# Performance work log

Hardware: AMD Instinct MI355X
Metric: run time of the kernel (lower is better)

The kernel has to match this reference:

```python
import jax, jax.numpy as jnp
import numpy as np
import math

D_MODEL = 1024
N_HEADS = 16
D_HEAD = D_MODEL // N_HEADS
LSR_RANK = 32
B, T = 4, 2048


def setup_inputs() -> dict:
    key = jax.random.key(0)
    ks = jax.random.split(key, 11)
    s = 1.0 / math.sqrt(D_MODEL)
    x = jax.random.normal(ks[0], (B, T, D_MODEL), dtype=jnp.float32)
    Wq = jax.random.uniform(ks[1], (D_MODEL, D_MODEL), minval=-s, maxval=s)
    bq = jax.random.uniform(ks[2], (D_MODEL,), minval=-s, maxval=s)
    Wk = jax.random.uniform(ks[3], (D_MODEL, D_MODEL), minval=-s, maxval=s)
    bk = jax.random.uniform(ks[4], (D_MODEL,), minval=-s, maxval=s)
    Wv = jax.random.uniform(ks[5], (D_MODEL, D_MODEL), minval=-s, maxval=s)
    bv = jax.random.uniform(ks[6], (D_MODEL,), minval=-s, maxval=s)
    Wo = jax.random.uniform(ks[7], (D_MODEL, D_MODEL), minval=-s, maxval=s)
    bo = jax.random.uniform(ks[8], (D_MODEL,), minval=-s, maxval=s)
    Wq_lsr = jax.random.normal(ks[9], (N_HEADS, D_HEAD, LSR_RANK)) / math.sqrt(D_HEAD)
    Wk_lsr = jax.random.normal(ks[10], (N_HEADS, D_HEAD, LSR_RANK)) / math.sqrt(D_HEAD)
    return {"x": x, "Wq": Wq, "bq": bq, "Wk": Wk, "bk": bk,
            "Wv": Wv, "bv": bv, "Wo": Wo, "bo": bo,
            "Wq_lsr": Wq_lsr, "Wk_lsr": Wk_lsr}


def reference(x, Wq, bq, Wk, bk, Wv, bv, Wo, bo, Wq_lsr, Wk_lsr):
    Bq, Tq, _ = x.shape
    # Linear projections (torch Linear: x @ W.T + b), split into heads -> (B,H,T,Dh)
    def split_heads(y):
        return y.reshape(Bq, Tq, N_HEADS, D_HEAD).transpose(0, 2, 1, 3)
    q = split_heads(x @ Wq.T + bq)
    k = split_heads(x @ Wk.T + bk)
    v = split_heads(x @ Wv.T + bv)
    # LSR: project q,k to rank-R per head
    q_lr = jnp.einsum('bhtd,hdr->bhtr', q, Wq_lsr)
    k_lr = jnp.einsum('bhtd,hdr->bhtr', k, Wk_lsr)
    scale = 1.0 / math.sqrt(max(LSR_RANK, 1))
    scores = jnp.einsum('bhir,bhjr->bhij', q_lr, k_lr) * scale  # (B,H,T,T)
    causal_mask = jnp.triu(jnp.ones((Tq, Tq), dtype=bool), k=1)
    scores = jnp.where(causal_mask, jnp.float32(-jnp.inf), scores)
    attn = jax.nn.softmax(scores, axis=-1)
    y = jnp.einsum('bhij,bhjd->bhid', attn, v)  # (B,H,T,Dh)
    y = y.transpose(0, 2, 1, 3).reshape(Bq, Tq, D_MODEL)
    return y @ Wo.T + bo
```

## Files before the change

kernel.cpp:

```cpp
#include <hip/hip_runtime.h>

#define B_  4
#define T_  2048
#define H_  16
#define DM_ 1024
#define DH_ 64
#define RK_ 32

using u16 = unsigned short;
using u32 = unsigned int;
typedef float  floatx4 __attribute__((ext_vector_type(4)));
typedef __bf16 bf16x8  __attribute__((ext_vector_type(8)));
typedef u16    u16x8   __attribute__((ext_vector_type(8)));
typedef u16    u16x4   __attribute__((ext_vector_type(4)));
typedef short  s16x4   __attribute__((ext_vector_type(4)));

#define MFMA16(a,b,c) __builtin_amdgcn_mfma_f32_16x16x32_bf16((a),(b),(c),0,0,0)
#define MFMA1K(a,b,c) __builtin_amdgcn_mfma_f32_16x16x16bf16_1k((a),(b),(c),0,0,0)

__device__ __forceinline__ u16 f2bf(float f) {
  unsigned u = __float_as_uint(f);
  u += 0x7fffu + ((u >> 16) & 1u);
  return (u16)(u >> 16);
}
__device__ __forceinline__ u32 pack_bf(float a, float b) {
  u32 ua = __float_as_uint(a); ua += 0x7fffu + ((ua >> 16) & 1u);
  u32 ub = __float_as_uint(b); ub += 0x7fffu + ((ub >> 16) & 1u);
  return __builtin_amdgcn_perm(ub, ua, 0x07060302u);
}
__device__ __forceinline__ u32 tpack(float a, float b) {
  return __builtin_amdgcn_perm(__float_as_uint(b), __float_as_uint(a), 0x07060302u);
}

__device__ __forceinline__ void async_copy16(const u16* g, const u16* lds_uniform_base) {
  __builtin_amdgcn_global_load_lds(
      (const __attribute__((address_space(1))) unsigned int*)(unsigned long long)g,
      (__attribute__((address_space(3))) unsigned int*)(unsigned int)(unsigned long long)lds_uniform_base,
      16, 0, 0);
}

__global__ __launch_bounds__(256) void cvt_x(const float* __restrict__ s,
                                             u16* __restrict__ d, int n4) {
  int i = blockIdx.x * 256 + threadIdx.x;
  if (i >= n4) return;
  float4 v = reinterpret_cast<const float4*>(s)[i];
  u16x4 o = { f2bf(v.x), f2bf(v.y), f2bf(v.z), f2bf(v.w) };
  reinterpret_cast<u16x4*>(d)[i] = o;
}

__global__ __launch_bounds__(256) void cvt_wvo(const float* __restrict__ Wv,
                                               const float* __restrict__ Wo,
                                               u16* __restrict__ Wcat) {
  int i = blockIdx.x * 256 + threadIdx.x;
  int reg = i >> 18;
  const float* s = reg ? Wo : Wv;
  int j = i & 262143;
  float4 v = reinterpret_cast<const float4*>(s)[j];
  u16x4 o = { f2bf(v.x), f2bf(v.y), f2bf(v.z), f2bf(v.w) };
  reinterpret_cast<u16x4*>(Wcat)[(reg ? 524288 : 0) + j] = o;
}

__global__ __launch_bounds__(256) void lsr_fold(const float* __restrict__ W,
                                                const float* __restrict__ bias,
                                                const float* __restrict__ lsr,
                                                float fold,
                                                u16* __restrict__ Weff,
                                                float* __restrict__ beff) {
  const int hr = blockIdx.x;
  const int h = hr >> 5, r = hr & 31;
  const int tid = threadIdx.x;
  __shared__ float lw[64];
  if (tid < 64) lw[tid] = lsr[(size_t)(h * 64 + tid) * 32 + r] * fold;
  __syncthreads();
  float a0 = 0.f, a1 = 0.f, a2 = 0.f, a3 = 0.f;
  for (int d = 0; d < 64; d++) {
    float l = lw[d];
    float4 wv = *reinterpret_cast<const float4*>(W + (size_t)(h * 64 + d) * 1024 + tid * 4);
    a0 += l * wv.x; a1 += l * wv.y; a2 += l * wv.z; a3 += l * wv.w;
  }
  u16x4 o = { f2bf(a0), f2bf(a1), f2bf(a2), f2bf(a3) };
  reinterpret_cast<u16x4*>(Weff)[(size_t)hr * 256 + tid] = o;
  if (tid == 0) {
    float s = 0.f;
    for (int d = 0; d < 64; d++) s += lw[d] * bias[h * 64 + d];
    beff[hr] = s;
  }
}

template <int MODE>
__global__ __launch_bounds__(256, 2) void gemm8(const u16* __restrict__ A,
                                                const u16* __restrict__ W,
                                                const float* __restrict__ b0,
                                                const float* __restrict__ b1,
                                                const float* __restrict__ b2,
                                                void* __restrict__ Cv,
                                                u16* __restrict__ qo,
                                                u16* __restrict__ ko,
                                                int ldc) {
  __shared__ __align__(16) u16 Al[2][8192];
  __shared__ __align__(16) u16 Bl[2][8192];
  const int tid  = threadIdx.x;
  const int lane = tid & 63;
  const int w    = tid >> 6;
  const int quad = lane >> 4;
  const int l16  = lane & 15;
  const int wm   = (w >> 1) << 6;
  const int wn   = (w & 1) << 6;

  const int bm = blockIdx.x << 7;
  const int bn = blockIdx.y << 7;

  const int sr = tid >> 3;
  const int sc = ((tid & 7) ^ (sr & 7)) * 8;
  const u16* Ag = A + (size_t)(bm + sr) * 1024 + sc;
  const u16* Wg = W + (size_t)(bn + sr) * 1024 + sc;

  auto stage = [&](int k0, int bsel) {
#pragma unroll
    for (int j = 0; j < 4; j++)
      async_copy16(Ag + (size_t)j * 32768 + k0, &Al[bsel][j * 2048 + w * 512]);
#pragma unroll
    for (int j = 0; j < 4; j++)
      async_copy16(Wg + (size_t)j * 32768 + k0, &Bl[bsel][j * 2048 + w * 512]);
  };

  int aoff[4], boff[4], sl[2];
#pragma unroll
  for (int mi = 0; mi < 4; mi++) aoff[mi] = (wm + mi * 16 + l16) * 64;
#pragma unroll
  for (int ni = 0; ni < 4; ni++) boff[ni] = (wn + ni * 16 + l16) * 64;
  sl[0] = ((0 + quad) ^ (l16 & 7)) * 8;
  sl[1] = ((4 + quad) ^ (l16 & 7)) * 8;

  floatx4 acc[4][4];
#pragma unroll
  for (int i = 0; i < 4; i++)
#pragma unroll
    for (int j = 0; j < 4; j++) acc[i][j] = (floatx4){0.f, 0.f, 0.f, 0.f};

  stage(0, 0);
  asm volatile("s_waitcnt vmcnt(0)" ::: "memory");
  __builtin_amdgcn_s_barrier();
  asm volatile("" ::: "memory");

  for (int i = 0; i < 16; i++) {
    if (i < 15) stage((i + 1) * 64, (i + 1) & 1);
    const u16* Ab = Al[i & 1];
    const u16* Bb = Bl[i & 1];
#pragma unroll
    for (int ks = 0; ks < 2; ks++) {
      bf16x8 af[4], bfr[4];
#pragma unroll
      for (int mi = 0; mi < 4; mi++)
        af[mi] = *reinterpret_cast<const bf16x8*>(Ab + aoff[mi] + sl[ks]);
#pragma unroll
      for (int ni = 0; ni < 4; ni++)
        bfr[ni] = *reinterpret_cast<const bf16x8*>(Bb + boff[ni] + sl[ks]);
      __builtin_amdgcn_s_setprio(1);
#pragma unroll
      for (int mi = 0; mi < 4; mi++)
#pragma unroll
        for (int ni = 0; ni < 4; ni++)
          acc[mi][ni] = MFMA16(af[mi], bfr[ni], acc[mi][ni]);
      __builtin_amdgcn_s_setprio(0);
    }
    if (i < 15) {
      asm volatile("s_waitcnt vmcnt(0)" ::: "memory");
      __builtin_amdgcn_s_barrier();
      asm volatile("" ::: "memory");
    }
  }

  if (MODE == 1) {
#pragma unroll
    for (int ni = 0; ni < 4; ni++) {
      int col = bn + wn + ni * 16 + l16;
      float bias = b0[col & 1023];
#pragma unroll
      for (int mi = 0; mi < 4; mi++)
#pragma unroll
        for (int r = 0; r < 4; r++) {
          int row = bm + wm + mi * 16 + quad * 4 + r;
          reinterpret_cast<float*>(Cv)[(size_t)row * ldc + col] = acc[mi][ni][r] + bias;
        }
    }
  } else {
    if (bn < 1024) {
#pragma unroll
      for (int ni = 0; ni < 4; ni++) {
        int col = bn + wn + ni * 16 + l16;
        float bias = b0[col];
#pragma unroll
        for (int mi = 0; mi < 4; mi++)
#pragma unroll
          for (int r = 0; r < 4; r++) {
            int row = bm + wm + mi * 16 + quad * 4 + r;
            reinterpret_cast<u16*>(Cv)[(size_t)row * 1024 + col] =
                f2bf(acc[mi][ni][r] + bias);
          }
      }
    } else {
      u16* outp = (bn < 1536) ? qo : ko;
      const float* bp = (bn < 1536) ? b1 : b2;
#pragma unroll
      for (int ni = 0; ni < 4; ni++) {
        int cc = (bn + wn + ni * 16 + l16) & 511;
        float bias = bp[cc];
        int hh = cc >> 5, rk = cc & 31;
#pragma unroll
        for (int mi = 0; mi < 4; mi++)
#pragma unroll
          for (int r = 0; r < 4; r++) {
            int row = bm + wm + mi * 16 + quad * 4 + r;
            size_t addr =
                ((size_t)((row >> 11) * 16 + hh) * 2048 + (row & 2047)) * 32 + rk;
            outp[addr] = f2bf(acc[mi][ni][r] + bias);
          }
      }
    }
  }
}

__global__ __launch_bounds__(256) void vtrans(const u16* __restrict__ V,
                                              u16* __restrict__ vt) {
  const int tb = blockIdx.x;
  const int bh = blockIdx.y;
  const int b = bh >> 4, h = bh & 15;
  __shared__ u16 Vl[64][72];
  const int tid = threadIdx.x;
#pragma unroll
  for (int it = 0; it < 2; it++) {
    int c = it * 256 + tid;
    int t = c >> 3, dc = (c & 7) * 8;
    u16x8 v = *reinterpret_cast<const u16x8*>(
        V + (size_t)(b * T_ + tb * 64 + t) * 1024 + h * 64 + dc);
    *reinterpret_cast<u16x8*>(&Vl[t][dc]) = v;
  }
  __syncthreads();
#pragma unroll
  for (int it = 0; it < 2; it++) {
    int c = it * 256 + tid;
    int d = c >> 3, tt = (c & 7) * 8;
    u16x8 o;
#pragma unroll
    for (int j = 0; j < 8; j++) o[j] = Vl[tt + j][d];
    *reinterpret_cast<u16x8*>(vt + ((size_t)bh * 64 + d) * T_ + tb * 64 + tt) = o;
  }
}

__global__ __launch_bounds__(256, 2) void attn(const u16* __restrict__ qlr,
                                               const u16* __restrict__ klr,
                                               const u16* __restrict__ vt,
                                               u16* __restrict__ yatt) {
  const int bh = blockIdx.x;
  const int b = bh >> 4, h = bh & 15;
  const int p = blockIdx.y;
  const int tid = threadIdx.x, lane = tid & 63, w = tid >> 6;
  const int quad = lane >> 4, l16 = lane & 15;

  __shared__ __align__(16) u16 Vt3[3][4096];
  __shared__ __align__(16) u16 Kt3[3][2048];

  const u16* qlr_bh = qlr + (size_t)bh * T_ * RK_;
  const u16* klr_bh = klr + (size_t)bh * T_ * RK_;
  const u16* vt_bh  = vt + (size_t)bh * 64 * T_;

  int voff[4][4];
#pragma unroll
  for (int nt = 0; nt < 4; nt++)
#pragma unroll
    for (int dt = 0; dt < 4; dt++) {
      int d = dt * 16 + l16;
      voff[nt][dt] = d * 64 + (((nt * 2 + (quad >> 1)) ^ (d & 7)) * 8) + (quad & 1) * 4;
    }
  int soffV[2];
#pragma unroll
  for (int issue = 0; issue < 2; issue++) {
    int L = issue * 256 + tid;
    int d = L >> 3, cg = L & 7;
    soffV[issue] = d * T_ + ((cg ^ (d & 7)) * 8);
  }
  const int soffK = (w * 8 + (lane >> 3)) * 64 + (((lane & 7) ^ (lane >> 3)) * 8);
  const int koff = (l16 >> 1) * 64 + ((((l16 & 1) * 4 + quad) ^ (l16 >> 1)) * 8);
  const int wub = w * 512;

  const floatx4 fzero = {0.f, 0.f, 0.f, 0.f};
  const int thrq = w * 16 + l16;

  for (int run = 0; run < 2; run++) {
    const int j = run ? p : 15 - p;
    const int q0 = j << 7;
    const int nfull = 2 * j;
    if (run) __syncthreads();

    bf16x8 qf[2];
#pragma unroll
    for (int qg = 0; qg < 2; qg++)
      qf[qg] = *reinterpret_cast<const bf16x8*>(
          qlr_bh + (size_t)(q0 + qg * 64 + thrq) * 32 + quad * 8);

    auto stage = [&](int t, int bi) {
      const u16* vs = vt_bh + t * 64;
      async_copy16(vs + soffV[0], &Vt3[bi][wub]);
      async_copy16(vs + soffV[1], &Vt3[bi][2048 + wub]);
      async_copy16(klr_bh + t * 2048 + soffK, &Kt3[bi][wub]);
    };

    stage(0, 0);
    stage(1, 1);
    asm volatile("s_waitcnt vmcnt(3)" ::: "memory");
    __builtin_amdgcn_s_barrier();
    asm volatile("" ::: "memory");

    floatx4 oacc[4][2];
#pragma unroll
    for (int i = 0; i < 4; i++)
#pragma unroll
      for (int jg = 0; jg < 2; jg++) oacc[i][jg] = fzero;
    float rs[2] = {0.f, 0.f};

    const u16* Vb = &Vt3[0][0];
    const u16* Kb = &Kt3[0][0];
    int cb = 0, sb = 2;

    for (int i = 0; i < nfull; i++) {
      stage(i + 2, sb);

      bf16x8 kf[4];
#pragma unroll
      for (int nt = 0; nt < 4; nt++)
        kf[nt] = *reinterpret_cast<const bf16x8*>(Kb + koff + nt * 512);

      uint2 pk[4][2];
#pragma unroll
      for (int qg = 0; qg < 2; qg++) {
        __builtin_amdgcn_s_setprio(1);
        floatx4 sv[4];
#pragma unroll
        for (int nt = 0; nt < 4; nt++) sv[nt] = MFMA16(kf[nt], qf[qg], fzero);
        __builtin_amdgcn_s_setprio(0);
#pragma unroll
        for (int nt = 0; nt < 4; nt++) {
          float p0 = __builtin_amdgcn_exp2f(sv[nt][0]);
          float p1 = __builtin_amdgcn_exp2f(sv[nt][1]);
          float p2 = __builtin_amdgcn_exp2f(sv[nt][2]);
          float p3 = __builtin_amdgcn_exp2f(sv[nt][3]);
          rs[qg] += (p0 + p1) + (p2 + p3);
          pk[nt][qg].x = tpack(p0, p1);
          pk[nt][qg].y = tpack(p2, p3);
        }
      }
      __builtin_amdgcn_s_setprio(1);
#pragma unroll
      for (int dt = 0; dt < 4; dt++)
#pragma unroll
        for (int nt = 0; nt < 4; nt++) {
          s16x4 vf = *reinterpret_cast<const s16x4*>(Vb + voff[nt][dt]);
          oacc[dt][0] = MFMA1K(vf, __builtin_bit_cast(s16x4, pk[nt][0]), oacc[dt][0]);
          oacc[dt][1] = MFMA1K(vf, __builtin_bit_cast(s16x4, pk[nt][1]), oacc[dt][1]);
        }
      __builtin_amdgcn_s_setprio(0);

      asm volatile("s_waitcnt vmcnt(3)" ::: "memory");
      __builtin_amdgcn_s_barrier();
      asm volatile("" ::: "memory");

      cb = (cb == 2) ? 0 : cb + 1;
      Vb = &Vt3[cb][0];
      Kb = &Kt3[cb][0];
      sb = (sb == 2) ? 0 : sb + 1;
    }

    {
      bf16x8 kf[4];
#pragma unroll
      for (int nt = 0; nt < 4; nt++)
        kf[nt] = *reinterpret_cast<const bf16x8*>(Kb + koff + nt * 512);

      uint2 pk[4][2];
#pragma unroll
      for (int nt = 0; nt < 4; nt++) {
        floatx4 sv = MFMA16(kf[nt], qf[0], fzero);
        const int keyl = nt * 16 + quad * 4;
        float pr[4];
#pragma unroll
        for (int r = 0; r < 4; r++) {
          float e = __builtin_amdgcn_exp2f(sv[r]);
          pr[r] = (keyl + r <= thrq) ? e : 0.f;
        }
        rs[0] += (pr[0] + pr[1]) + (pr[2] + pr[3]);
        pk[nt][0].x = tpack(pr[0], pr[1]);
        pk[nt][0].y = tpack(pr[2], pr[3]);
      }
#pragma unroll
      for (int nt = 0; nt < 4; nt++) {
        floatx4 sv = MFMA16(kf[nt], qf[1], fzero);
        float p0 = __builtin_amdgcn_exp2f(sv[0]);
        float p1 = __builtin_amdgcn_exp2f(sv[1]);
        float p2 = __builtin_amdgcn_exp2f(sv[2]);
        float p3 = __builtin_amdgcn_exp2f(sv[3]);
        rs[1] += (p0 + p1) + (p2 + p3);
        pk[nt][1].x = tpack(p0, p1);
        pk[nt][1].y = tpack(p2, p3);
      }
      __builtin_amdgcn_s_setprio(1);
#pragma unroll
      for (int dt = 0; dt < 4; dt++)
#pragma unroll
        for (int nt = 0; nt < 4; nt++) {
          s16x4 vf = *reinterpret_cast<const s16x4*>(Vb + voff[nt][dt]);
          oacc[dt][0] = MFMA1K(vf, __builtin_bit_cast(s16x4, pk[nt][0]), oacc[dt][0]);
          oacc[dt][1] = MFMA1K(vf, __builtin_bit_cast(s16x4, pk[nt][1]), oacc[dt][1]);
        }
      __builtin_amdgcn_s_setprio(0);

      asm volatile("s_waitcnt vmcnt(0)" ::: "memory");
      __builtin_amdgcn_s_barrier();
      asm volatile("" ::: "memory");

      cb = (cb == 2) ? 0 : cb + 1;
      Vb = &Vt3[cb][0];
      Kb = &Kt3[cb][0];
    }

    {
      bf16x8 kf[4];
#pragma unroll
      for (int nt = 0; nt < 4; nt++)
        kf[nt] = *reinterpret_cast<const bf16x8*>(Kb + koff + nt * 512);

      uint2 pk[4];
#pragma unroll
      for (int nt = 0; nt < 4; nt++) {
        floatx4 sv = MFMA16(kf[nt], qf[1], fzero);
        const int keyl = nt * 16 + quad * 4;
        float pr[4];
#pragma unroll
        for (int r = 0; r < 4; r++) {
          float e = __builtin_amdgcn_exp2f(sv[r]);
          pr[r] = (keyl + r <= thrq) ? e : 0.f;
        }
        rs[1] += (pr[0] + pr[1]) + (pr[2] + pr[3]);
        pk[nt].x = tpack(pr[0], pr[1]);
        pk[nt].y = tpack(pr[2], pr[3]);
      }
      __builtin_amdgcn_s_setprio(1);
#pragma unroll
      for (int dt = 0; dt < 4; dt++)
#pragma unroll
        for (int nt = 0; nt < 4; nt++) {
          s16x4 vf = *reinterpret_cast<const s16x4*>(Vb + voff[nt][dt]);
          oacc[dt][1] = MFMA1K(vf, __builtin_bit_cast(s16x4, pk[nt]), oacc[dt][1]);
        }
      __builtin_amdgcn_s_setprio(0);
    }

#pragma unroll
    for (int qg = 0; qg < 2; qg++) {
      rs[qg] += __shfl_xor(rs[qg], 16);
      rs[qg] += __shfl_xor(rs[qg], 32);
    }
#pragma unroll
    for (int qg = 0; qg < 2; qg++) {
      float inv = 1.f / rs[qg];
      const int qrow = q0 + qg * 64 + thrq;
#pragma unroll
      for (int dt = 0; dt < 4; dt++) {
        uint2 ov = { pack_bf(oacc[dt][qg][0] * inv, oacc[dt][qg][1] * inv),
                     pack_bf(oacc[dt][qg][2] * inv, oacc[dt][qg][3] * inv) };
        *reinterpret_cast<uint2*>(
            yatt + (size_t)(b * T_ + qrow) * 1024 + h * 64 + dt * 16 + quad * 4) = ov;
      }
    }
  }
}

extern "C" void kernel_launch(void* const* d_in, const int* in_sizes, int n_in,
                              void* d_out, int out_size, void* d_ws, size_t ws_size,
                              hipStream_t stream) {
  const float* x   = (const float*)d_in[0];
  const float* Wq  = (const float*)d_in[1];
  const float* bq  = (const float*)d_in[2];
  const float* Wk  = (const float*)d_in[3];
  const float* bk  = (const float*)d_in[4];
  const float* Wv  = (const float*)d_in[5];
  const float* bv  = (const float*)d_in[6];
  const float* Wo  = (const float*)d_in[7];
  const float* bo  = (const float*)d_in[8];
  const float* Wql = (const float*)d_in[9];
  const float* Wkl = (const float*)d_in[10];
  float* out = (float*)d_out;

  char* ws = (char*)d_ws;
  u16*   xb    = (u16*)(ws);
  u16*   Wcat  = (u16*)(ws + 16777216);
  float* beffq = (float*)(ws + 23068672);
  float* beffk = (float*)(ws + 23072768);
  u16*   Vbuf  = (u16*)(ws + 25165824);
  u16*   qlr   = (u16*)(ws + 41943040);
  u16*   klr   = (u16*)(ws + 50331648);
  u16*   yatt  = (u16*)(ws + 58720256);
  u16*   vt    = xb;

  const float foldq = 0.25506100790944405f;

  cvt_x<<<dim3(8192), 256, 0, stream>>>(x, xb, 2097152);
  cvt_wvo<<<dim3(2048), 256, 0, stream>>>(Wv, Wo, Wcat);
  lsr_fold<<<dim3(512), 256, 0, stream>>>(Wq, bq, Wql, foldq, Wcat + 1048576, beffq);
  lsr_fold<<<dim3(512), 256, 0, stream>>>(Wk, bk, Wkl, 1.0f, Wcat + 1572864, beffk);
  gemm8<2><<<dim3(64, 16), 256, 0, stream>>>(xb, Wcat, bv, beffq, beffk,
                                             Vbuf, qlr, klr, 0);
  vtrans<<<dim3(32, 64), 256, 0, stream>>>(Vbuf, vt);
  attn<<<dim3(64, 8), 256, 0, stream>>>(qlr, klr, vt, yatt);
  gemm8<1><<<dim3(64, 8), 256, 0, stream>>>(yatt, Wcat + 2097152, bo, bo, bo,
                                            out, nullptr, nullptr, 1024);
}
```

Before: 242.9 us.

## Use 128-key double-buffered tiles in attention and merge weight-prep kernels

```diff
diff --git a/kernel.cpp b/kernel.cpp
--- a/kernel.cpp
+++ b/kernel.cpp
@@ -48,28 +48,39 @@
   reinterpret_cast<u16x4*>(d)[i] = o;
 }
 
-__global__ __launch_bounds__(256) void cvt_wvo(const float* __restrict__ Wv,
-                                               const float* __restrict__ Wo,
-                                               u16* __restrict__ Wcat) {
-  int i = blockIdx.x * 256 + threadIdx.x;
-  int reg = i >> 18;
-  const float* s = reg ? Wo : Wv;
-  int j = i & 262143;
-  float4 v = reinterpret_cast<const float4*>(s)[j];
-  u16x4 o = { f2bf(v.x), f2bf(v.y), f2bf(v.z), f2bf(v.w) };
-  reinterpret_cast<u16x4*>(Wcat)[(reg ? 524288 : 0) + j] = o;
-}
-
-__global__ __launch_bounds__(256) void lsr_fold(const float* __restrict__ W,
-                                                const float* __restrict__ bias,
-                                                const float* __restrict__ lsr,
-                                                float fold,
-                                                u16* __restrict__ Weff,
-                                                float* __restrict__ beff) {
-  const int hr = blockIdx.x;
+__global__ __launch_bounds__(256) void prep_w(const float* __restrict__ Wv,
+                                              const float* __restrict__ Wo,
+                                              const float* __restrict__ Wq,
+                                              const float* __restrict__ bq,
+                                              const float* __restrict__ Wql,
+                                              const float* __restrict__ Wk,
+                                              const float* __restrict__ bk,
+                                              const float* __restrict__ Wkl,
+                                              u16* __restrict__ Wcat,
+                                              float* __restrict__ beffq,
+                                              float* __restrict__ beffk) {
+  const int tid = threadIdx.x;
+  const int bid = blockIdx.x;
+  __shared__ float lw[64];
+  if (bid < 2048) {
+    int i = bid * 256 + tid;
+    int reg = i >> 18;
+    const float* s = reg ? Wo : Wv;
+    int j = i & 262143;
+    float4 v = reinterpret_cast<const float4*>(s)[j];
+    u16x4 o = { f2bf(v.x), f2bf(v.y), f2bf(v.z), f2bf(v.w) };
+    reinterpret_cast<u16x4*>(Wcat)[(reg ? 524288 : 0) + j] = o;
+    return;
+  }
+  const int sel = (bid >= 2560);
+  const int hr = bid - (sel ? 2560 : 2048);
   const int h = hr >> 5, r = hr & 31;
-  const int tid = threadIdx.x;
-  __shared__ float lw[64];
+  const float* W    = sel ? Wk : Wq;
+  const float* bias = sel ? bk : bq;
+  const float* lsr  = sel ? Wkl : Wql;
+  const float fold  = sel ? 1.0f : 0.25506100790944405f;
+  u16*   Weff = Wcat + (sel ? 1572864 : 1048576);
+  float* beff = sel ? beffk : beffq;
   if (tid < 64) lw[tid] = lsr[(size_t)(h * 64 + tid) * 32 + r] * fold;
   __syncthreads();
   float a0 = 0.f, a1 = 0.f, a2 = 0.f, a3 = 0.f;
@@ -258,30 +269,33 @@
   const int tid = threadIdx.x, lane = tid & 63, w = tid >> 6;
   const int quad = lane >> 4, l16 = lane & 15;
 
-  __shared__ __align__(16) u16 Vt3[3][4096];
-  __shared__ __align__(16) u16 Kt3[3][2048];
+  __shared__ __align__(16) u16 Vt2[2][8192];
+  __shared__ __align__(16) u16 Kt2[2][4096];
 
   const u16* qlr_bh = qlr + (size_t)bh * T_ * RK_;
   const u16* klr_bh = klr + (size_t)bh * T_ * RK_;
   const u16* vt_bh  = vt + (size_t)bh * 64 * T_;
 
-  int voff[4][4];
-#pragma unroll
-  for (int nt = 0; nt < 4; nt++)
-#pragma unroll
-    for (int dt = 0; dt < 4; dt++) {
-      int d = dt * 16 + l16;
-      voff[nt][dt] = d * 64 + (((nt * 2 + (quad >> 1)) ^ (d & 7)) * 8) + (quad & 1) * 4;
-    }
-  int soffV[2];
-#pragma unroll
-  for (int issue = 0; issue < 2; issue++) {
-    int L = issue * 256 + tid;
-    int d = L >> 3, cg = L & 7;
-    soffV[issue] = d * T_ + ((cg ^ (d & 7)) * 8);
-  }
-  const int soffK = (w * 8 + (lane >> 3)) * 64 + (((lane & 7) ^ (lane >> 3)) * 8);
+  int voffN[8];
+#pragma unroll
+  for (int nt = 0; nt < 8; nt++)
+    voffN[nt] = l16 * 128 + (((nt * 2 + (quad >> 1)) ^ l16) * 8) + (quad & 1) * 4;
   const int koff = (l16 >> 1) * 64 + ((((l16 & 1) * 4 + quad) ^ (l16 >> 1)) * 8);
+
+  int soffV[4];
+#pragma unroll
+  for (int it = 0; it < 4; it++) {
+    int L = it * 256 + tid;
+    int d = L >> 4, s = L & 15;
+    soffV[it] = d * T_ + ((s ^ (d & 15)) * 8);
+  }
+  int soffK[2];
+#pragma unroll
+  for (int it = 0; it < 2; it++) {
+    int L = it * 256 + tid;
+    int pr = L >> 3, s = L & 7;
+    soffK[it] = pr * 64 + ((s ^ (pr & 7)) * 8);
+  }
   const int wub = w * 512;
 
   const floatx4 fzero = {0.f, 0.f, 0.f, 0.f};
@@ -290,8 +304,7 @@
   for (int run = 0; run < 2; run++) {
     const int j = run ? p : 15 - p;
     const int q0 = j << 7;
-    const int nfull = 2 * j;
-    if (run) __syncthreads();
+    const int nkt = j + 1;
 
     bf16x8 qf[2];
 #pragma unroll
@@ -300,15 +313,16 @@
           qlr_bh + (size_t)(q0 + qg * 64 + thrq) * 32 + quad * 8);
 
     auto stage = [&](int t, int bi) {
-      const u16* vs = vt_bh + t * 64;
-      async_copy16(vs + soffV[0], &Vt3[bi][wub]);
-      async_copy16(vs + soffV[1], &Vt3[bi][2048 + wub]);
-      async_copy16(klr_bh + t * 2048 + soffK, &Kt3[bi][wub]);
+#pragma unroll
+      for (int it = 0; it < 4; it++)
+        async_copy16(vt_bh + t * 128 + soffV[it], &Vt2[bi][it * 2048 + wub]);
+#pragma unroll
+      for (int it = 0; it < 2; it++)
+        async_copy16(klr_bh + t * 4096 + soffK[it], &Kt2[bi][it * 2048 + wub]);
     };
 
     stage(0, 0);
-    stage(1, 1);
-    asm volatile("s_waitcnt vmcnt(3)" ::: "memory");
+    asm volatile("s_waitcnt vmcnt(0)" ::: "memory");
     __builtin_amdgcn_s_barrier();
     asm volatile("" ::: "memory");
 
@@ -319,140 +333,72 @@
       for (int jg = 0; jg < 2; jg++) oacc[i][jg] = fzero;
     float rs[2] = {0.f, 0.f};
 
-    const u16* Vb = &Vt3[0][0];
-    const u16* Kb = &Kt3[0][0];
-    int cb = 0, sb = 2;
-
-    for (int i = 0; i < nfull; i++) {
-      stage(i + 2, sb);
-
-      bf16x8 kf[4];
-#pragma unroll
-      for (int nt = 0; nt < 4; nt++)
+    for (int i = 0; i < nkt; i++) {
+      const bool last = (i == nkt - 1);
+      if (!last) stage(i + 1, (i + 1) & 1);
+      const u16* Vb = &Vt2[i & 1][0];
+      const u16* Kb = &Kt2[i & 1][0];
+
+      bf16x8 kf[8];
+#pragma unroll
+      for (int nt = 0; nt < 8; nt++)
         kf[nt] = *reinterpret_cast<const bf16x8*>(Kb + koff + nt * 512);
 
-      uint2 pk[4][2];
-#pragma unroll
-      for (int qg = 0; qg < 2; qg++) {
-        __builtin_amdgcn_s_setprio(1);
-        floatx4 sv[4];
-#pragma unroll
-        for (int nt = 0; nt < 4; nt++) sv[nt] = MFMA16(kf[nt], qf[qg], fzero);
-        __builtin_amdgcn_s_setprio(0);
-#pragma unroll
-        for (int nt = 0; nt < 4; nt++) {
-          float p0 = __builtin_amdgcn_exp2f(sv[nt][0]);
-          float p1 = __builtin_amdgcn_exp2f(sv[nt][1]);
-          float p2 = __builtin_amdgcn_exp2f(sv[nt][2]);
-          float p3 = __builtin_amdgcn_exp2f(sv[nt][3]);
-          rs[qg] += (p0 + p1) + (p2 + p3);
-          pk[nt][qg].x = tpack(p0, p1);
-          pk[nt][qg].y = tpack(p2, p3);
+      uint2 pk[8][2];
+      if (!last) {
+#pragma unroll
+        for (int qg = 0; qg < 2; qg++) {
+          __builtin_amdgcn_s_setprio(1);
+          floatx4 sv[8];
+#pragma unroll
+          for (int nt = 0; nt < 8; nt++) sv[nt] = MFMA16(kf[nt], qf[qg], fzero);
+          __builtin_amdgcn_s_setprio(0);
+#pragma unroll
+          for (int nt = 0; nt < 8; nt++) {
+            float p0 = __builtin_amdgcn_exp2f(sv[nt][0]);
+            float p1 = __builtin_amdgcn_exp2f(sv[nt][1]);
+            float p2 = __builtin_amdgcn_exp2f(sv[nt][2]);
+            float p3 = __builtin_amdgcn_exp2f(sv[nt][3]);
+            rs[qg] += (p0 + p1) + (p2 + p3);
+            pk[nt][qg].x = tpack(p0, p1);
+            pk[nt][qg].y = tpack(p2, p3);
+          }
+        }
+      } else {
+#pragma unroll
+        for (int qg = 0; qg < 2; qg++) {
+          const int thr = qg * 64 + thrq;
+#pragma unroll
+          for (int nt = 0; nt < 8; nt++) {
+            floatx4 sv = MFMA16(kf[nt], qf[qg], fzero);
+            const int keyl = nt * 16 + quad * 4;
+            float pr[4];
+#pragma unroll
+            for (int r = 0; r < 4; r++) {
+              float e = __builtin_amdgcn_exp2f(sv[r]);
+              pr[r] = (keyl + r <= thr) ? e : 0.f;
+            }
+            rs[qg] += (pr[0] + pr[1]) + (pr[2] + pr[3]);
+            pk[nt][qg].x = tpack(pr[0], pr[1]);
+            pk[nt][qg].y = tpack(pr[2], pr[3]);
+          }
         }
       }
+
       __builtin_amdgcn_s_setprio(1);
 #pragma unroll
       for (int dt = 0; dt < 4; dt++)
 #pragma unroll
-        for (int nt = 0; nt < 4; nt++) {
-          s16x4 vf = *reinterpret_cast<const s16x4*>(Vb + voff[nt][dt]);
+        for (int nt = 0; nt < 8; nt++) {
+          s16x4 vf = *reinterpret_cast<const s16x4*>(Vb + voffN[nt] + dt * 2048);
           oacc[dt][0] = MFMA1K(vf, __builtin_bit_cast(s16x4, pk[nt][0]), oacc[dt][0]);
           oacc[dt][1] = MFMA1K(vf, __builtin_bit_cast(s16x4, pk[nt][1]), oacc[dt][1]);
         }
       __builtin_amdgcn_s_setprio(0);
 
-      asm volatile("s_waitcnt vmcnt(3)" ::: "memory");
-      __builtin_amdgcn_s_barrier();
-      asm volatile("" ::: "memory");
-
-      cb = (cb == 2) ? 0 : cb + 1;
-      Vb = &Vt3[cb][0];
-      Kb = &Kt3[cb][0];
-      sb = (sb == 2) ? 0 : sb + 1;
-    }
-
-    {
-      bf16x8 kf[4];
-#pragma unroll
-      for (int nt = 0; nt < 4; nt++)
-        kf[nt] = *reinterpret_cast<const bf16x8*>(Kb + koff + nt * 512);
-
-      uint2 pk[4][2];
-#pragma unroll
-      for (int nt = 0; nt < 4; nt++) {
-        floatx4 sv = MFMA16(kf[nt], qf[0], fzero);
-        const int keyl = nt * 16 + quad * 4;
-        float pr[4];
-#pragma unroll
-        for (int r = 0; r < 4; r++) {
-          float e = __builtin_amdgcn_exp2f(sv[r]);
-          pr[r] = (keyl + r <= thrq) ? e : 0.f;
-        }
-        rs[0] += (pr[0] + pr[1]) + (pr[2] + pr[3]);
-        pk[nt][0].x = tpack(pr[0], pr[1]);
-        pk[nt][0].y = tpack(pr[2], pr[3]);
-      }
-#pragma unroll
-      for (int nt = 0; nt < 4; nt++) {
-        floatx4 sv = MFMA16(kf[nt], qf[1], fzero);
-        float p0 = __builtin_amdgcn_exp2f(sv[0]);
-        float p1 = __builtin_amdgcn_exp2f(sv[1]);
-        float p2 = __builtin_amdgcn_exp2f(sv[2]);
-        float p3 = __builtin_amdgcn_exp2f(sv[3]);
-        rs[1] += (p0 + p1) + (p2 + p3);
-        pk[nt][1].x = tpack(p0, p1);
-        pk[nt][1].y = tpack(p2, p3);
-      }
-      __builtin_amdgcn_s_setprio(1);
-#pragma unroll
-      for (int dt = 0; dt < 4; dt++)
-#pragma unroll
-        for (int nt = 0; nt < 4; nt++) {
-          s16x4 vf = *reinterpret_cast<const s16x4*>(Vb + voff[nt][dt]);
-          oacc[dt][0] = MFMA1K(vf, __builtin_bit_cast(s16x4, pk[nt][0]), oacc[dt][0]);
-          oacc[dt][1] = MFMA1K(vf, __builtin_bit_cast(s16x4, pk[nt][1]), oacc[dt][1]);
-        }
-      __builtin_amdgcn_s_setprio(0);
-
       asm volatile("s_waitcnt vmcnt(0)" ::: "memory");
       __builtin_amdgcn_s_barrier();
       asm volatile("" ::: "memory");
-
-      cb = (cb == 2) ? 0 : cb + 1;
-      Vb = &Vt3[cb][0];
-      Kb = &Kt3[cb][0];
-    }
-
-    {
-      bf16x8 kf[4];
-#pragma unroll
-      for (int nt = 0; nt < 4; nt++)
-        kf[nt] = *reinterpret_cast<const bf16x8*>(Kb + koff + nt * 512);
-
-      uint2 pk[4];
-#pragma unroll
-      for (int nt = 0; nt < 4; nt++) {
-        floatx4 sv = MFMA16(kf[nt], qf[1], fzero);
-        const int keyl = nt * 16 + quad * 4;
-        float pr[4];
-#pragma unroll
-        for (int r = 0; r < 4; r++) {
-          float e = __builtin_amdgcn_exp2f(sv[r]);
-          pr[r] = (keyl + r <= thrq) ? e : 0.f;
-        }
-        rs[1] += (pr[0] + pr[1]) + (pr[2] + pr[3]);
-        pk[nt].x = tpack(pr[0], pr[1]);
-        pk[nt].y = tpack(pr[2], pr[3]);
-      }
-      __builtin_amdgcn_s_setprio(1);
-#pragma unroll
-      for (int dt = 0; dt < 4; dt++)
-#pragma unroll
-        for (int nt = 0; nt < 4; nt++) {
-          s16x4 vf = *reinterpret_cast<const s16x4*>(Vb + voff[nt][dt]);
-          oacc[dt][1] = MFMA1K(vf, __builtin_bit_cast(s16x4, pk[nt]), oacc[dt][1]);
-        }
-      __builtin_amdgcn_s_setprio(0);
     }
 
 #pragma unroll
@@ -502,12 +448,9 @@
   u16*   yatt  = (u16*)(ws + 58720256);
   u16*   vt    = xb;
 
-  const float foldq = 0.25506100790944405f;
-
   cvt_x<<<dim3(8192), 256, 0, stream>>>(x, xb, 2097152);
-  cvt_wvo<<<dim3(2048), 256, 0, stream>>>(Wv, Wo, Wcat);
-  lsr_fold<<<dim3(512), 256, 0, stream>>>(Wq, bq, Wql, foldq, Wcat + 1048576, beffq);
-  lsr_fold<<<dim3(512), 256, 0, stream>>>(Wk, bk, Wkl, 1.0f, Wcat + 1572864, beffk);
+  prep_w<<<dim3(3072), 256, 0, stream>>>(Wv, Wo, Wq, bq, Wql, Wk, bk, Wkl,
+                                         Wcat, beffq, beffk);
   gemm8<2><<<dim3(64, 16), 256, 0, stream>>>(xb, Wcat, bv, beffq, beffk,
                                              Vbuf, qlr, klr, 0);
   vtrans<<<dim3(32, 64), 256, 0, stream>>>(Vbuf, vt);
```

Measured after the change: 234.5 us. 3.5% less time.
